# Performance work log

Measured on AMD Instinct MI355X. Metric: run time of the kernel, lower is better.

## Reference

```python
import jax, jax.numpy as jnp
import numpy as np

H, L, D, R = 16, 4096, 64, 128   # heads, seq len, head dim, FAVOR+ feature dim
S_SCALE = 0.125                  # attention inner-product scaling S
CHUNK = 128                      # chunk size for causal linear attention
EPS = 1e-10                      # module's self.epsilon denominator guard


def _get_proj(d, r, seed=0):
    # get_proj(R, D, orthogonal=True, hyperbolic=True): QR-orthogonalized
    # Gaussian block rescaled by chi column norms, then [W, -W].
    rng = np.random.RandomState(seed)
    rh = r // 2
    w = rng.randn(d, rh)
    chis = np.linalg.norm(w, ord=2, axis=0, keepdims=True)
    qm, _ = np.linalg.qr(w, mode='reduced')
    w = qm * chis
    return np.concatenate((w, -w), axis=1).astype(np.float32)  # (D, R)


def setup_inputs() -> dict:
    key = jax.random.key(0)
    kq, kk, kv = jax.random.split(key, 3)
    q = jax.random.normal(kq, (H, L, D), dtype=jnp.float32)
    k = jax.random.normal(kk, (H, L, D), dtype=jnp.float32)
    v = jax.random.normal(kv, (H, L, D), dtype=jnp.float32)
    W = jnp.asarray(_get_proj(D, R))
    return {"T": 64, "k": k, "q": q, "v": v, "W": W}


def _phi(x, W):
    # FAVOR+ feature map: x' = x * S^0.5 / D^0.25;
    # phi(x) = exp(W^T x' - ||x'||^2 / 2) / sqrt(R)
    xs = x * (S_SCALE ** 0.5 / D ** 0.25)            # (H, L, D)
    Wx = jnp.einsum('hld,dr->hlr', xs, W)            # (H, L, R)
    sq = 0.5 * jnp.sum(xs * xs, axis=-1, keepdims=True)
    return jnp.exp(Wx - sq) / (R ** 0.5)             # (H, L, R)


def reference(T, k, q, v, W):
    # Deterministic FAVOR+ estimator of the strictly-causal softmax attention
    # Pred_l = sum_{j<l} v_j exp(S<q_l,k_j>) / sum_{i<l} exp(S<q_l,k_i>)
    # which the tree+sampling machinery approximates (T = sampling budget,
    # irrelevant for the exact kernel estimate). Chunked linear attention.
    del T
    pq = _phi(q, W)                                  # (H, L, R)
    pk = _phi(k, W)                                  # (H, L, R)
    nc = L // CHUNK
    pq_c = pq.reshape(H, nc, CHUNK, R)
    pk_c = pk.reshape(H, nc, CHUNK, R)
    v_c = v.reshape(H, nc, CHUNK, D)
    # per-chunk KV summaries and exclusive prefix over chunks
    skv = jnp.einsum('hncr,hncd->hnrd', pk_c, v_c)   # (H, nc, R, D)
    zk = jnp.sum(pk_c, axis=2)                       # (H, nc, R)
    skv_prev = jnp.cumsum(skv, axis=1) - skv         # exclusive
    zk_prev = jnp.cumsum(zk, axis=1) - zk
    num_inter = jnp.einsum('hncr,hnrd->hncd', pq_c, skv_prev)
    den_inter = jnp.einsum('hncr,hnr->hnc', pq_c, zk_prev)
    # intra-chunk strictly-causal part (j < l)
    A = jnp.einsum('hncr,hnsr->hncs', pq_c, pk_c)    # (H, nc, C, C)
    mask = jnp.tril(jnp.ones((CHUNK, CHUNK), dtype=A.dtype), k=-1)
    A = A * mask
    num_intra = jnp.einsum('hncs,hnsd->hncd', A, v_c)
    den_intra = jnp.sum(A, axis=-1)
    out = (num_inter + num_intra) / (den_inter + den_intra + EPS)[..., None]
    return out.reshape(H, L, D)
```

## Files before the change

### kernel.cpp

```cpp
#include <hip/hip_runtime.h>

#define H 16
#define L 4096
#define D 64
#define R 128
#define C2 64
#define NC2 64
#define HN2 (H * NC2)
#define EPS 1e-10f
#define XS_SCALE 0.125f
#define PHI_SCALE 0.08838834764831845f

typedef __attribute__((ext_vector_type(8))) short bf8;
typedef __attribute__((ext_vector_type(4))) short bf4;
typedef __attribute__((ext_vector_type(16))) float facc16;

static __device__ __forceinline__ unsigned short f2b(float f) {
    unsigned u = __float_as_uint(f);
    return (unsigned short)((u + 0x7fffu + ((u >> 16) & 1u)) >> 16);
}
static __device__ __forceinline__ float b2f(unsigned short s) {
    return __uint_as_float(((unsigned)s) << 16);
}

__global__ __launch_bounds__(256) void kW(const float* __restrict__ W,
                                          unsigned short* __restrict__ Wtg) {
    for (int i = threadIdx.x; i < 8192; i += 256) {
        int d = i >> 7, r = i & 127;
        Wtg[(unsigned)((r * 64 + d) ^ ((r & 7) << 3))] = f2b(W[i]);
    }
}

__global__ __launch_bounds__(256) void k1(
    const float* __restrict__ q, const float* __restrict__ k,
    const float* __restrict__ v, const unsigned short* __restrict__ Wtg,
    unsigned short* __restrict__ pq, unsigned short* __restrict__ pk,
    unsigned short* __restrict__ vTg, unsigned short* __restrict__ skvTp,
    float* __restrict__ zk)
{
    __shared__ __align__(16) unsigned short A_[8192];
    __shared__ __align__(16) unsigned short B_[4096];
    __shared__ __align__(16) unsigned short C_[8192];
    const int tid = threadIdx.x, hn = blockIdx.x;
    const int lane = tid & 63, wave = tid >> 6, lo = lane & 31, hi = lane >> 5;
    const int rg = wave & 1, ch = wave >> 1;
    const size_t cbase = (size_t)hn * C2 * D;

    for (int i = tid; i < 1024; i += 256)
        *(bf8*)&A_[i * 8] = *(const bf8*)(Wtg + i * 8);
    for (int i = tid; i < 1024; i += 256) {
        int row = i >> 4, d0 = (i & 15) * 4;
        float4 vv = *(const float4*)(q + cbase + row * 64 + d0);
        unsigned* p = (unsigned*)&B_[(unsigned)((row * 64 + d0) ^ ((row & 7) << 3))];
        p[0] = (unsigned)f2b(vv.x * XS_SCALE) | ((unsigned)f2b(vv.y * XS_SCALE) << 16);
        p[1] = (unsigned)f2b(vv.z * XS_SCALE) | ((unsigned)f2b(vv.w * XS_SCALE) << 16);
    }
    __syncthreads();

    {
        bf8 af[4]; float ssq = 0.f;
        #pragma unroll
        for (int s = 0; s < 4; ++s) {
            af[s] = *(const bf8*)&B_[(unsigned)(((rg * 32 + lo) * 64 + 16 * s + 8 * hi) ^ ((lo & 7) << 3))];
            #pragma unroll
            for (int e = 0; e < 8; ++e) { float t = b2f((unsigned short)af[s][e]); ssq += t * t; }
        }
        ssq += __shfl_xor(ssq, 32); ssq *= 0.5f;
        float sqrow[16];
        #pragma unroll
        for (int reg = 0; reg < 16; ++reg)
            sqrow[reg] = __shfl(ssq, (reg & 3) + 8 * (reg >> 2) + 4 * hi);
        facc16 acc[2];
        #pragma unroll
        for (int t = 0; t < 2; ++t)
            #pragma unroll
            for (int e = 0; e < 16; ++e) acc[t][e] = 0.f;
        #pragma unroll
        for (int s = 0; s < 4; ++s)
            #pragma unroll
            for (int t = 0; t < 2; ++t) {
                const bf8 b = *(const bf8*)&A_[(unsigned)((((2 * ch + t) * 32 + lo) * 64 + 16 * s + 8 * hi) ^ ((lo & 7) << 3))];
                acc[t] = __builtin_amdgcn_mfma_f32_32x32x16_bf16(af[s], b, acc[t], 0, 0, 0);
            }
        #pragma unroll
        for (int t = 0; t < 2; ++t)
            #pragma unroll
            for (int reg = 0; reg < 16; ++reg) {
                int row = rg * 32 + (reg & 3) + 8 * (reg >> 2) + 4 * hi;
                int col = (2 * ch + t) * 32 + lo;
                C_[(unsigned)((row * 128 + col) ^ ((row & 15) << 3))] =
                    f2b(__expf(acc[t][reg] - sqrow[reg]) * PHI_SCALE);
            }
    }
    __syncthreads();

    for (int i = tid; i < 1024; i += 256)
        *(bf8*)(pq + (size_t)hn * 8192 + i * 8) = *(const bf8*)&C_[i * 8];
    for (int i = tid; i < 1024; i += 256) {
        int row = i >> 4, d0 = (i & 15) * 4;
        float4 vv = *(const float4*)(k + cbase + row * 64 + d0);
        unsigned* p = (unsigned*)&B_[(unsigned)((row * 64 + d0) ^ ((row & 7) << 3))];
        p[0] = (unsigned)f2b(vv.x * XS_SCALE) | ((unsigned)f2b(vv.y * XS_SCALE) << 16);
        p[1] = (unsigned)f2b(vv.z * XS_SCALE) | ((unsigned)f2b(vv.w * XS_SCALE) << 16);
    }
    __syncthreads();

    facc16 acck[2];
    float sqk[16];
    {
        bf8 af[4]; float ssq = 0.f;
        #pragma unroll
        for (int s = 0; s < 4; ++s) {
            af[s] = *(const bf8*)&B_[(unsigned)(((rg * 32 + lo) * 64 + 16 * s + 8 * hi) ^ ((lo & 7) << 3))];
            #pragma unroll
            for (int e = 0; e < 8; ++e) { float t = b2f((unsigned short)af[s][e]); ssq += t * t; }
        }
        ssq += __shfl_xor(ssq, 32); ssq *= 0.5f;
        #pragma unroll
        for (int reg = 0; reg < 16; ++reg)
            sqk[reg] = __shfl(ssq, (reg & 3) + 8 * (reg >> 2) + 4 * hi);
        #pragma unroll
        for (int t = 0; t < 2; ++t)
            #pragma unroll
            for (int e = 0; e < 16; ++e) acck[t][e] = 0.f;
        #pragma unroll
        for (int s = 0; s < 4; ++s)
            #pragma unroll
            for (int t = 0; t < 2; ++t) {
                const bf8 b = *(const bf8*)&A_[(unsigned)((((2 * ch + t) * 32 + lo) * 64 + 16 * s + 8 * hi) ^ ((lo & 7) << 3))];
                acck[t] = __builtin_amdgcn_mfma_f32_32x32x16_bf16(af[s], b, acck[t], 0, 0, 0);
            }
    }
    __syncthreads();

    #pragma unroll
    for (int t = 0; t < 2; ++t) {
        int colr = (2 * ch + t) * 32 + lo;
        #pragma unroll
        for (int g = 0; g < 4; ++g) {
            int c0 = rg * 32 + 8 * g + 4 * hi;
            bf4 pk4;
            #pragma unroll
            for (int e = 0; e < 4; ++e) {
                unsigned short b = f2b(__expf(acck[t][4 * g + e] - sqk[4 * g + e]) * PHI_SCALE);
                pk4[e] = (short)b;
                C_[(unsigned)(((c0 + e) * 128 + colr) ^ (((c0 + e) & 15) << 3))] = b;
            }
            *(bf4*)&A_[(unsigned)((colr * 64 + c0) ^ ((colr & 7) << 3))] = pk4;
        }
    }
    __syncthreads();

    for (int i = tid; i < 1024; i += 256)
        *(bf8*)(pk + (size_t)hn * 8192 + i * 8) = *(const bf8*)&C_[i * 8];
    for (int i = tid; i < 4096; i += 256) {
        int d = i & 63, c = i >> 6;
        B_[(unsigned)((d * 64 + c) ^ ((d & 7) << 3))] = f2b(v[cbase + c * 64 + d]);
    }
    if (tid < 128) {
        float s = 0.f;
        #pragma unroll
        for (int j = 0; j < 8; ++j) {
            bf8 a8 = *(const bf8*)&A_[(unsigned)((tid * 64 + 8 * j) ^ ((tid & 7) << 3))];
            #pragma unroll
            for (int e = 0; e < 8; ++e) s += b2f((unsigned short)a8[e]);
        }
        zk[(size_t)hn * 128 + tid] = s;
    }
    __syncthreads();

    for (int i = tid; i < 512; i += 256)
        *(bf8*)(vTg + (size_t)hn * 4096 + i * 8) = *(const bf8*)&B_[i * 8];
    {
        facc16 acs[2];
        #pragma unroll
        for (int t = 0; t < 2; ++t)
            #pragma unroll
            for (int e = 0; e < 16; ++e) acs[t][e] = 0.f;
        #pragma unroll
        for (int s = 0; s < 4; ++s) {
            const bf8 a = *(const bf8*)&B_[(unsigned)(((rg * 32 + lo) * 64 + 16 * s + 8 * hi) ^ ((lo & 7) << 3))];
            #pragma unroll
            for (int t = 0; t < 2; ++t) {
                const bf8 b = *(const bf8*)&A_[(unsigned)((((2 * ch + t) * 32 + lo) * 64 + 16 * s + 8 * hi) ^ ((lo & 7) << 3))];
                acs[t] = __builtin_amdgcn_mfma_f32_32x32x16_bf16(a, b, acs[t], 0, 0, 0);
            }
        }
        unsigned short* sg = skvTp + (size_t)hn * 8192;
        #pragma unroll
        for (int t = 0; t < 2; ++t)
            #pragma unroll
            for (int reg = 0; reg < 16; ++reg) {
                int d = rg * 32 + (reg & 3) + 8 * (reg >> 2) + 4 * hi;
                int r = (2 * ch + t) * 32 + lo;
                sg[d * 128 + r] = f2b(acs[t][reg]);
            }
    }
}

__global__ __launch_bounds__(256) void k2(unsigned short* __restrict__ skvTp,
                                          const float* __restrict__ zk,
                                          unsigned short* __restrict__ zkp)
{
    const int bid = blockIdx.x, tid = threadIdx.x;
    if (bid < 512) {
        int g = bid * 256 + tid;
        int h = g >> 13, dr = g & 8191;
        unsigned short* p = skvTp + (size_t)h * NC2 * 8192 + dr;
        float run = 0.f;
        #pragma unroll
        for (int n = 0; n < NC2; ++n) {
            float t = b2f(p[(size_t)n * 8192]);
            p[(size_t)n * 8192] = f2b(run);
            run += t;
        }
    } else {
        int g2 = (bid - 512) * 256 + tid;
        int h = g2 >> 7, r = g2 & 127;
        const float* pz = zk + (size_t)h * NC2 * 128 + r;
        unsigned short* oz = zkp + (size_t)h * NC2 * 128 + r;
        float run = 0.f;
        #pragma unroll
        for (int n = 0; n < NC2; ++n) {
            float t = pz[n * 128];
            oz[n * 128] = f2b(run);
            run += t;
        }
    }
}

__global__ __launch_bounds__(256) void k3(
    const unsigned short* __restrict__ pq, const unsigned short* __restrict__ pk,
    const unsigned short* __restrict__ vTg, const unsigned short* __restrict__ skvTp,
    const unsigned short* __restrict__ zkp, float* __restrict__ out)
{
    __shared__ __align__(16) unsigned short P_[8192];
    __shared__ __align__(16) unsigned short Q_[8192];
    __shared__ __align__(16) unsigned short V_[4096];
    const int tid = threadIdx.x, hn = blockIdx.x;
    const int lane = tid & 63, wave = tid >> 6, lo = lane & 31, hi = lane >> 5;
    const int rg = wave & 1, ch = wave >> 1;

    for (int i = tid; i < 1024; i += 256)
        *(bf8*)&P_[i * 8] = *(const bf8*)(pq + (size_t)hn * 8192 + i * 8);
    for (int i = tid; i < 1024; i += 256)
        *(bf8*)&Q_[i * 8] = *(const bf8*)(pk + (size_t)hn * 8192 + i * 8);
    for (int i = tid; i < 512; i += 256)
        *(bf8*)&V_[i * 8] = *(const bf8*)(vTg + (size_t)hn * 4096 + i * 8);
    __syncthreads();

    bf8 qf[8];
    #pragma unroll
    for (int s = 0; s < 8; ++s)
        qf[s] = *(const bf8*)&P_[(unsigned)(((rg * 32 + lo) * 128 + 16 * s + 8 * hi) ^ ((lo & 15) << 3))];
    __syncthreads();

    for (int i = tid; i < 1024; i += 256) {
        bf8 t8 = *(const bf8*)(skvTp + (size_t)hn * 8192 + i * 8);
        int d = i >> 4, r0 = (i & 15) * 8;
        *(bf8*)&P_[(unsigned)((d * 128 + r0) ^ ((d & 15) << 3))] = t8;
    }
    bf8 onesf, zf[8];
    #pragma unroll
    for (int e = 0; e < 8; ++e) onesf[e] = (lo == 0) ? (short)0x3F80 : (short)0;
    #pragma unroll
    for (int s = 0; s < 8; ++s)
        #pragma unroll
        for (int e = 0; e < 8; ++e) zf[s][e] = 0;
    if (lo == 0) {
        #pragma unroll
        for (int s = 0; s < 8; ++s)
            zf[s] = *(const bf8*)(zkp + (size_t)hn * 128 + 16 * s + 8 * hi);
    }

    facc16 ac1;
    #pragma unroll
    for (int e = 0; e < 16; ++e) ac1[e] = 0.f;
    #pragma unroll
    for (int s = 0; s < 8; ++s) {
        const bf8 b = *(const bf8*)&Q_[(unsigned)(((ch * 32 + lo) * 128 + 16 * s + 8 * hi) ^ ((lo & 15) << 3))];
        ac1 = __builtin_amdgcn_mfma_f32_32x32x16_bf16(qf[s], b, ac1, 0, 0, 0);
    }
    __syncthreads();

    #pragma unroll
    for (int reg = 0; reg < 16; ++reg) {
        int row = rg * 32 + (reg & 3) + 8 * (reg >> 2) + 4 * hi;
        int sc = ch * 32 + lo;
        Q_[(unsigned)((row * 64 + sc) ^ ((row & 7) << 3))] = f2b(sc < row ? ac1[reg] : 0.f);
    }
    __syncthreads();

    facc16 an, ad;
    #pragma unroll
    for (int e = 0; e < 16; ++e) { an[e] = 0.f; ad[e] = 0.f; }
    #pragma unroll
    for (int s = 0; s < 4; ++s) {
        const bf8 a = *(const bf8*)&Q_[(unsigned)(((rg * 32 + lo) * 64 + 16 * s + 8 * hi) ^ ((lo & 7) << 3))];
        const bf8 b = *(const bf8*)&V_[(unsigned)(((ch * 32 + lo) * 64 + 16 * s + 8 * hi) ^ ((lo & 7) << 3))];
        an = __builtin_amdgcn_mfma_f32_32x32x16_bf16(a, b, an, 0, 0, 0);
        ad = __builtin_amdgcn_mfma_f32_32x32x16_bf16(a, onesf, ad, 0, 0, 0);
    }
    #pragma unroll
    for (int s = 0; s < 8; ++s) {
        const bf8 b = *(const bf8*)&P_[(unsigned)(((ch * 32 + lo) * 128 + 16 * s + 8 * hi) ^ ((lo & 15) << 3))];
        an = __builtin_amdgcn_mfma_f32_32x32x16_bf16(qf[s], b, an, 0, 0, 0);
        ad = __builtin_amdgcn_mfma_f32_32x32x16_bf16(qf[s], zf[s], ad, 0, 0, 0);
    }
    float* og = out + (size_t)hn * C2 * D;
    #pragma unroll
    for (int reg = 0; reg < 16; ++reg) {
        int row = rg * 32 + (reg & 3) + 8 * (reg >> 2) + 4 * hi;
        float dv = __shfl(ad[reg], lane & 32);
        og[row * 64 + ch * 32 + lo] = an[reg] / (dv + EPS);
    }
}

extern "C" void kernel_launch(void* const* d_in, const int* in_sizes, int n_in,
                              void* d_out, int out_size, void* d_ws, size_t ws_size,
                              hipStream_t stream) {
    const float* k = (const float*)d_in[1];
    const float* q = (const float*)d_in[2];
    const float* v = (const float*)d_in[3];
    const float* W = (const float*)d_in[4];
    float* out = (float*)d_out;

    unsigned short* pq    = (unsigned short*)d_ws;
    unsigned short* pk    = pq + (size_t)HN2 * 8192;
    unsigned short* vTg   = pk + (size_t)HN2 * 8192;
    unsigned short* skvTp = vTg + (size_t)HN2 * 4096;
    unsigned short* Wtg   = skvTp + (size_t)HN2 * 8192;
    unsigned short* zkp   = Wtg + 8192;
    float* zk             = (float*)(zkp + (size_t)HN2 * 128);

    kW<<<1, 256, 0, stream>>>(W, Wtg);
    k1<<<HN2, 256, 0, stream>>>(q, k, v, Wtg, pq, pk, vTg, skvTp, zk);
    k2<<<520, 256, 0, stream>>>(skvTp, zk, zkp);
    k3<<<HN2, 256, 0, stream>>>(pq, pk, vTg, skvTp, zkp, out);
}
```

Before: 64.63 us.

## Prefetch k/v early, transpose v via identity MFMA, batch scan loads

k1 now issues the k and v global loads into registers well before they are needed, so their latency overlaps with the earlier MFMA phases. The strided scalar transpose of v into shared memory is replaced by coalesced float4 loads plus an identity-matrix MFMA that performs the transpose. k2 loads all 64 chunk values of its scan into registers up front instead of alternating each load with a store. A minBlocks=4 launch bound is added to k1; together with the extra live registers this raises register pressure and the risk of spills.

```diff
diff --git a/kernel.cpp b/kernel.cpp
--- a/kernel.cpp
+++ b/kernel.cpp
@@ -31,7 +31,7 @@
     }
 }
 
-__global__ __launch_bounds__(256) void k1(
+__global__ __launch_bounds__(256, 4) void k1(
     const float* __restrict__ q, const float* __restrict__ k,
     const float* __restrict__ v, const unsigned short* __restrict__ Wtg,
     unsigned short* __restrict__ pq, unsigned short* __restrict__ pk,
@@ -45,13 +45,19 @@
     const int lane = tid & 63, wave = tid >> 6, lo = lane & 31, hi = lane >> 5;
     const int rg = wave & 1, ch = wave >> 1;
     const size_t cbase = (size_t)hn * C2 * D;
-
+    const int prow = tid >> 4, pd0 = (tid & 15) * 4;
+
+    float4 kv4[4];
+    #pragma unroll
+    for (int n = 0; n < 4; ++n)
+        kv4[n] = *(const float4*)(k + cbase + (prow + 16 * n) * 64 + pd0);
     for (int i = tid; i < 1024; i += 256)
         *(bf8*)&A_[i * 8] = *(const bf8*)(Wtg + i * 8);
-    for (int i = tid; i < 1024; i += 256) {
-        int row = i >> 4, d0 = (i & 15) * 4;
-        float4 vv = *(const float4*)(q + cbase + row * 64 + d0);
-        unsigned* p = (unsigned*)&B_[(unsigned)((row * 64 + d0) ^ ((row & 7) << 3))];
+    #pragma unroll
+    for (int n = 0; n < 4; ++n) {
+        int row = prow + 16 * n;
+        float4 vv = *(const float4*)(q + cbase + row * 64 + pd0);
+        unsigned* p = (unsigned*)&B_[(unsigned)((row * 64 + pd0) ^ ((row & 7) << 3))];
         p[0] = (unsigned)f2b(vv.x * XS_SCALE) | ((unsigned)f2b(vv.y * XS_SCALE) << 16);
         p[1] = (unsigned)f2b(vv.z * XS_SCALE) | ((unsigned)f2b(vv.w * XS_SCALE) << 16);
     }
@@ -94,14 +100,18 @@
     }
     __syncthreads();
 
+    float4 vv4[4];
+    #pragma unroll
+    for (int n = 0; n < 4; ++n)
+        vv4[n] = *(const float4*)(v + cbase + (prow + 16 * n) * 64 + pd0);
     for (int i = tid; i < 1024; i += 256)
         *(bf8*)(pq + (size_t)hn * 8192 + i * 8) = *(const bf8*)&C_[i * 8];
-    for (int i = tid; i < 1024; i += 256) {
-        int row = i >> 4, d0 = (i & 15) * 4;
-        float4 vv = *(const float4*)(k + cbase + row * 64 + d0);
-        unsigned* p = (unsigned*)&B_[(unsigned)((row * 64 + d0) ^ ((row & 7) << 3))];
-        p[0] = (unsigned)f2b(vv.x * XS_SCALE) | ((unsigned)f2b(vv.y * XS_SCALE) << 16);
-        p[1] = (unsigned)f2b(vv.z * XS_SCALE) | ((unsigned)f2b(vv.w * XS_SCALE) << 16);
+    #pragma unroll
+    for (int n = 0; n < 4; ++n) {
+        int row = prow + 16 * n;
+        unsigned* p = (unsigned*)&B_[(unsigned)((row * 64 + pd0) ^ ((row & 7) << 3))];
+        p[0] = (unsigned)f2b(kv4[n].x * XS_SCALE) | ((unsigned)f2b(kv4[n].y * XS_SCALE) << 16);
+        p[1] = (unsigned)f2b(kv4[n].z * XS_SCALE) | ((unsigned)f2b(kv4[n].w * XS_SCALE) << 16);
     }
     __syncthreads();
 
@@ -149,14 +159,17 @@
             *(bf4*)&A_[(unsigned)((colr * 64 + c0) ^ ((colr & 7) << 3))] = pk4;
         }
     }
+    #pragma unroll
+    for (int n = 0; n < 4; ++n) {
+        int row = prow + 16 * n;
+        unsigned* p = (unsigned*)&B_[(unsigned)((row * 64 + pd0) ^ ((row & 7) << 3))];
+        p[0] = (unsigned)f2b(vv4[n].x) | ((unsigned)f2b(vv4[n].y) << 16);
+        p[1] = (unsigned)f2b(vv4[n].z) | ((unsigned)f2b(vv4[n].w) << 16);
+    }
     __syncthreads();
 
     for (int i = tid; i < 1024; i += 256)
         *(bf8*)(pk + (size_t)hn * 8192 + i * 8) = *(const bf8*)&C_[i * 8];
-    for (int i = tid; i < 4096; i += 256) {
-        int d = i & 63, c = i >> 6;
-        B_[(unsigned)((d * 64 + c) ^ ((d & 7) << 3))] = f2b(v[cbase + c * 64 + d]);
-    }
     if (tid < 128) {
         float s = 0.f;
         #pragma unroll
@@ -167,10 +180,41 @@
         }
         zk[(size_t)hn * 128 + tid] = s;
     }
+    bf8 aid[2];
+    #pragma unroll
+    for (int s2 = 0; s2 < 2; ++s2)
+        #pragma unroll
+        for (int e = 0; e < 8; ++e)
+            aid[s2][e] = (e == lo - 16 * s2 - 8 * hi) ? (short)0x3F80 : (short)0;
+    facc16 tv[2][2];
+    #pragma unroll
+    for (int t = 0; t < 2; ++t)
+        #pragma unroll
+        for (int u = 0; u < 2; ++u) {
+            #pragma unroll
+            for (int e = 0; e < 16; ++e) tv[t][u][e] = 0.f;
+            #pragma unroll
+            for (int s2 = 0; s2 < 2; ++s2) {
+                const bf8 b = *(const bf8*)&B_[(unsigned)(((32 * u + lo) * 64 + 16 * (2 * t + s2) + 8 * hi) ^ ((lo & 7) << 3))];
+                tv[t][u] = __builtin_amdgcn_mfma_f32_32x32x16_bf16(aid[s2], b, tv[t][u], 0, 0, 0);
+            }
+        }
+    __syncthreads();
+
+    #pragma unroll
+    for (int t = 0; t < 2; ++t)
+        #pragma unroll
+        for (int u = 0; u < 2; ++u)
+            #pragma unroll
+            for (int reg = 0; reg < 16; ++reg) {
+                int d = 32 * t + (reg & 3) + 8 * (reg >> 2) + 4 * hi;
+                int c = 32 * u + lo;
+                C_[(unsigned)((d * 64 + c) ^ ((d & 7) << 3))] = f2b(tv[t][u][reg]);
+            }
     __syncthreads();
 
     for (int i = tid; i < 512; i += 256)
-        *(bf8*)(vTg + (size_t)hn * 4096 + i * 8) = *(const bf8*)&B_[i * 8];
+        *(bf8*)(vTg + (size_t)hn * 4096 + i * 8) = *(const bf8*)&C_[i * 8];
     {
         facc16 acs[2];
         #pragma unroll
@@ -179,7 +223,7 @@
             for (int e = 0; e < 16; ++e) acs[t][e] = 0.f;
         #pragma unroll
         for (int s = 0; s < 4; ++s) {
-            const bf8 a = *(const bf8*)&B_[(unsigned)(((rg * 32 + lo) * 64 + 16 * s + 8 * hi) ^ ((lo & 7) << 3))];
+            const bf8 a = *(const bf8*)&C_[(unsigned)(((rg * 32 + lo) * 64 + 16 * s + 8 * hi) ^ ((lo & 7) << 3))];
             #pragma unroll
             for (int t = 0; t < 2; ++t) {
                 const bf8 b = *(const bf8*)&A_[(unsigned)((((2 * ch + t) * 32 + lo) * 64 + 16 * s + 8 * hi) ^ ((lo & 7) << 3))];
@@ -207,10 +251,13 @@
         int g = bid * 256 + tid;
         int h = g >> 13, dr = g & 8191;
         unsigned short* p = skvTp + (size_t)h * NC2 * 8192 + dr;
+        unsigned short vals[NC2];
+        #pragma unroll
+        for (int n = 0; n < NC2; ++n) vals[n] = p[(size_t)n * 8192];
         float run = 0.f;
         #pragma unroll
         for (int n = 0; n < NC2; ++n) {
-            float t = b2f(p[(size_t)n * 8192]);
+            float t = b2f(vals[n]);
             p[(size_t)n * 8192] = f2b(run);
             run += t;
         }
@@ -219,12 +266,14 @@
         int h = g2 >> 7, r = g2 & 127;
         const float* pz = zk + (size_t)h * NC2 * 128 + r;
         unsigned short* oz = zkp + (size_t)h * NC2 * 128 + r;
+        float vals[NC2];
+        #pragma unroll
+        for (int n = 0; n < NC2; ++n) vals[n] = pz[n * 128];
         float run = 0.f;
         #pragma unroll
         for (int n = 0; n < NC2; ++n) {
-            float t = pz[n * 128];
             oz[n * 128] = f2b(run);
-            run += t;
+            run += vals[n];
         }
     }
 }
```

New measurement: 63.44 us. No clear change (-1.8%).
